# Optimization experiments

Measured on AMD Instinct MI355X. Metric: run time of the kernel, lower is better.

## Reference

```python
import math
import jax, jax.numpy as jnp
import numpy as np

HEADS = 9
EMBED = 32
TEMPERATURE = 3000.0

def _conv1x1(x, W, b):
    # x: [B,C,H,W], W: [O,C], b: [O]  (1x1 conv == channel matmul)
    return jnp.einsum('bchw,oc->bohw', x, W) + b[None, :, None, None]

def setup_inputs() -> dict:
    key = jax.random.key(0)
    ks = jax.random.split(key, 14)
    B, H, W = 2, 64, 64
    h2, w2 = 32, 32
    hd = HEADS * EMBED  # 288
    s = 0.1
    return {
        'second_frame': jax.random.normal(ks[0], (B, 3, H, W), jnp.float32),
        'first_frame_aligned': jax.random.normal(ks[1], (B, 3, H, W), jnp.float32),
        'second_frame_feat': jax.random.normal(ks[2], (B, 4, h2, w2), jnp.float32),
        'first_frame_feat_aligned': jax.random.normal(ks[3], (B, 4, h2, w2), jnp.float32),
        'Wq': jax.random.normal(ks[4], (hd, 3), jnp.float32) * s,
        'bq': jax.random.normal(ks[5], (hd,), jnp.float32) * s,
        'Wk': jax.random.normal(ks[6], (hd, 3), jnp.float32) * s,
        'bk': jax.random.normal(ks[7], (hd,), jnp.float32) * s,
        'Wv': jax.random.normal(ks[8], (hd, 4), jnp.float32) * s,
        'bv': jax.random.normal(ks[9], (hd,), jnp.float32) * s,
        'Wp': jax.random.normal(ks[10], (4, hd), jnp.float32) * s,
        'bp': jax.random.normal(ks[11], (4,), jnp.float32) * s,
        'Wt': jax.random.normal(ks[12], (1, EMBED), jnp.float32) * s,
        'bt': jax.random.normal(ks[13], (1,), jnp.float32) * s,
    }

def reference(second_frame, first_frame_aligned, second_frame_feat,
              first_frame_feat_aligned, Wq, bq, Wk, bk, Wv, bv, Wp, bp, Wt, bt):
    B, _, H, W = second_frame.shape
    HW = H * W
    # bilinear upsample of aligned features to (H, W); half-pixel centers == align_corners=False
    feat_up = jax.image.resize(first_frame_feat_aligned,
                               (B, first_frame_feat_aligned.shape[1], H, W),
                               method='linear', antialias=False)
    Q = _conv1x1(second_frame, Wq, bq).reshape(B, HEADS, EMBED, HW)
    K = _conv1x1(first_frame_aligned, Wk, bk).reshape(B, HEADS, EMBED, HW)
    V = _conv1x1(feat_up, Wv, bv).reshape(B, HEADS, EMBED, HW)
    Qn = jnp.transpose(Q, (0, 1, 3, 2))                      # [B,h,HW,d]
    sim = jnp.einsum('bhnd,bhdm->bhnm', Qn, K) / math.sqrt(EMBED)  # [B,h,HW,HW]
    # learned per-query threshold from Q
    t = jnp.einsum('bhnd,od->bhno', Qn, Wt) + bt             # [B,h,HW,1]
    attn = jax.nn.relu((sim - t) / TEMPERATURE)              # no row normalization
    out = jnp.einsum('bhnm,bhdm->bhnd', attn, V)             # [B,h,HW,d]
    out = jnp.transpose(out, (0, 1, 3, 2)).reshape(B, HEADS * EMBED, H, W)
    out_feat = _conv1x1(out, Wp, bp)                         # [B,4,H,W]
    h2, w2 = second_frame_feat.shape[-2:]
    out_feat_down = jax.image.resize(out_feat, (B, out_feat.shape[1], h2, w2),
                                     method='linear', antialias=False)
    final_feat = second_frame_feat + out_feat_down
    return final_feat, out_feat_down
```

## Files before the change

kernel.cpp:

```cpp
#include <hip/hip_runtime.h>
#include <hip/hip_bf16.h>
#include <cstddef>

#define NHEADS 9
#define D 32
#define SQ 4096
#define ZSPLIT 8
#define MBLK (SQ / ZSPLIT)
#define CHUNKS (MBLK / 64)
#define KROW 40
#define VROW 72

typedef __attribute__((ext_vector_type(8))) short bf16x8;
typedef __attribute__((ext_vector_type(4))) short bf16x4;
typedef __attribute__((ext_vector_type(4))) float f32x4;

__device__ __forceinline__ unsigned int f2bf(float f) {
    unsigned int u = __float_as_uint(f);
    u += 0x7fffu + ((u >> 16) & 1u);
    return u >> 16;
}

__device__ __forceinline__ void lds_barrier() {
    asm volatile("s_waitcnt lgkmcnt(0)\n\ts_barrier" ::: "memory");
}

__device__ __forceinline__ unsigned int trunc_pk(float lo, float hi) {
    return __builtin_amdgcn_perm(__float_as_uint(hi), __float_as_uint(lo),
                                 0x07060302u);
}

__device__ __forceinline__ bf16x8 relu_pack8(f32x4 s1, f32x4 s2) {
    const f32x4 zz = {0.f, 0.f, 0.f, 0.f};
    f32x4 a = __builtin_elementwise_max(s1, zz);
    f32x4 b = __builtin_elementwise_max(s2, zz);
    union { unsigned int u[4]; bf16x8 v; } P;
    P.u[0] = trunc_pk(a[0], a[1]);
    P.u[1] = trunc_pk(a[2], a[3]);
    P.u[2] = trunc_pk(b[0], b[1]);
    P.u[3] = trunc_pk(b[2], b[3]);
    return P.v;
}

__global__ __launch_bounds__(256) void prep_kernel(
    const float* __restrict__ x2, const float* __restrict__ x1,
    const float* __restrict__ feat1,
    const float* __restrict__ Wq, const float* __restrict__ bq,
    const float* __restrict__ Wk, const float* __restrict__ bk,
    const float* __restrict__ Wv, const float* __restrict__ bv,
    const float* __restrict__ Wt, const float* __restrict__ bt,
    unsigned short* __restrict__ Qb, unsigned short* __restrict__ Kb,
    unsigned short* __restrict__ Vt, float* __restrict__ tbuf,
    float* __restrict__ of)
{
    __shared__ unsigned short Vls[32 * 66];

    const int tid = threadIdx.x;
    int idx = blockIdx.x * blockDim.x + tid;
    if (idx < 2 * 4 * SQ) of[idx] = 0.0f;
    int g  = idx & 3;
    int nl = tid >> 2;
    int n  = (idx >> 2) & (SQ - 1);
    int bh = idx >> 14;
    int h  = bh % NHEADS;
    int b  = bh / NHEADS;

    float xs0 = x2[((size_t)b * 3 + 0) * SQ + n];
    float xs1 = x2[((size_t)b * 3 + 1) * SQ + n];
    float xs2 = x2[((size_t)b * 3 + 2) * SQ + n];
    float ys0 = x1[((size_t)b * 3 + 0) * SQ + n];
    float ys1 = x1[((size_t)b * 3 + 1) * SQ + n];
    float ys2 = x1[((size_t)b * 3 + 2) * SQ + n];

    int yy = n >> 6, xx = n & 63;
    int jy = yy >> 1, jx = xx >> 1;
    int j0, j1, i0, i1; float wy0, wy1, wx0, wx1;
    if (yy & 1) { j0 = jy; j1 = (jy < 31) ? jy + 1 : 31; wy0 = 0.75f; wy1 = 0.25f; }
    else        { j0 = (jy > 0) ? jy - 1 : 0; j1 = jy;   wy0 = 0.25f; wy1 = 0.75f; }
    if (xx & 1) { i0 = jx; i1 = (jx < 31) ? jx + 1 : 31; wx0 = 0.75f; wx1 = 0.25f; }
    else        { i0 = (jx > 0) ? jx - 1 : 0; i1 = jx;   wx0 = 0.25f; wx1 = 0.75f; }

    float fu[4];
#pragma unroll
    for (int c = 0; c < 4; ++c) {
        const float* f = feat1 + ((size_t)b * 4 + c) * 1024;
        fu[c] = wy0 * (wx0 * f[j0 * 32 + i0] + wx1 * f[j0 * 32 + i1]) +
                wy1 * (wx0 * f[j1 * 32 + i0] + wx1 * f[j1 * 32 + i1]);
    }

    const int d0 = g * 8;
    unsigned int qp[4], kp[4];
    float tpart = 0.0f;
#pragma unroll
    for (int j = 0; j < 8; ++j) {
        int d = d0 + j, hd = h * D + d;
        float q = bq[hd] + Wq[hd * 3] * xs0 + Wq[hd * 3 + 1] * xs1 + Wq[hd * 3 + 2] * xs2;
        float k = bk[hd] + Wk[hd * 3] * ys0 + Wk[hd * 3 + 1] * ys1 + Wk[hd * 3 + 2] * ys2;
        float v = bv[hd] + Wv[hd * 4] * fu[0] + Wv[hd * 4 + 1] * fu[1] +
                  Wv[hd * 4 + 2] * fu[2] + Wv[hd * 4 + 3] * fu[3];
        tpart += q * Wt[d];
        unsigned int qb_ = f2bf(q), kb_ = f2bf(k);
        if (j & 1) { qp[j >> 1] |= qb_ << 16; kp[j >> 1] |= kb_ << 16; }
        else       { qp[j >> 1]  = qb_;       kp[j >> 1]  = kb_; }
        Vls[d * 66 + nl] = (unsigned short)f2bf(v);
    }
    tpart += __shfl_xor(tpart, 1);
    tpart += __shfl_xor(tpart, 2);
    if (g == 0) tbuf[(size_t)bh * SQ + n] = tpart + bt[0];

    size_t base = ((size_t)bh * SQ + n) * D + d0;
    *(uint4*)(Qb + base) = make_uint4(qp[0], qp[1], qp[2], qp[3]);
    *(uint4*)(Kb + base) = make_uint4(kp[0], kp[1], kp[2], kp[3]);

    __syncthreads();
    {
        int r  = tid >> 3;
        int c4 = tid & 7;
        int n0 = (blockIdx.x & 63) * 64;
        unsigned int w0 = *(const unsigned int*)&Vls[r * 66 + c4 * 4];
        unsigned int w1 = *(const unsigned int*)&Vls[r * 66 + c4 * 4 + 2];
        *(uint2*)(Vt + ((size_t)bh * D + r) * SQ + n0 + c4 * 4) = make_uint2(w0, w1);
    }
}

#define COMPUTE(KS, VS)                                                          \
    {                                                                            \
        _Pragma("unroll")                                                        \
        for (int g32 = 0; g32 < 2; ++g32) {                                      \
            const unsigned short* kbase = KS + g32 * 32 * KROW;                  \
            bf16x8 kf1 = *(const bf16x8*)(kbase + l15 * KROW + quad * 8);        \
            bf16x8 kf2 = *(const bf16x8*)(kbase + (16 + l15) * KROW + quad * 8); \
            bf16x8 vlo = *(const bf16x8*)(VS + l15 * VROW + g32 * 32 + quad * 8);\
            bf16x8 vhi = *(const bf16x8*)(VS + (l15 + 16) * VROW + g32 * 32 + quad * 8);\
            f32x4 sA1 = __builtin_amdgcn_mfma_f32_16x16x32_bf16(kf1, qfA, ciA, 0, 0, 0);\
            f32x4 sA2 = __builtin_amdgcn_mfma_f32_16x16x32_bf16(kf2, qfA, ciA, 0, 0, 0);\
            f32x4 sB1 = __builtin_amdgcn_mfma_f32_16x16x32_bf16(kf1, qfB, ciB, 0, 0, 0);\
            f32x4 sB2 = __builtin_amdgcn_mfma_f32_16x16x32_bf16(kf2, qfB, ciB, 0, 0, 0);\
            f32x4 sC1 = __builtin_amdgcn_mfma_f32_16x16x32_bf16(kf1, qfC, ciC, 0, 0, 0);\
            f32x4 sC2 = __builtin_amdgcn_mfma_f32_16x16x32_bf16(kf2, qfC, ciC, 0, 0, 0);\
            f32x4 sD1 = __builtin_amdgcn_mfma_f32_16x16x32_bf16(kf1, qfD, ciD, 0, 0, 0);\
            f32x4 sD2 = __builtin_amdgcn_mfma_f32_16x16x32_bf16(kf2, qfD, ciD, 0, 0, 0);\
            bf16x8 pA = relu_pack8(sA1, sA2);                                    \
            bf16x8 pB = relu_pack8(sB1, sB2);                                    \
            bf16x8 pC = relu_pack8(sC1, sC2);                                    \
            bf16x8 pD = relu_pack8(sD1, sD2);                                    \
            accAl = __builtin_amdgcn_mfma_f32_16x16x32_bf16(vlo, pA, accAl, 0, 0, 0);\
            accAh = __builtin_amdgcn_mfma_f32_16x16x32_bf16(vhi, pA, accAh, 0, 0, 0);\
            accBl = __builtin_amdgcn_mfma_f32_16x16x32_bf16(vlo, pB, accBl, 0, 0, 0);\
            accBh = __builtin_amdgcn_mfma_f32_16x16x32_bf16(vhi, pB, accBh, 0, 0, 0);\
            accCl = __builtin_amdgcn_mfma_f32_16x16x32_bf16(vlo, pC, accCl, 0, 0, 0);\
            accCh = __builtin_amdgcn_mfma_f32_16x16x32_bf16(vhi, pC, accCh, 0, 0, 0);\
            accDl = __builtin_amdgcn_mfma_f32_16x16x32_bf16(vlo, pD, accDl, 0, 0, 0);\
            accDh = __builtin_amdgcn_mfma_f32_16x16x32_bf16(vhi, pD, accDh, 0, 0, 0);\
        }                                                                        \
    }

__global__ __launch_bounds__(256, 4) void attn_kernel(
    const unsigned short* __restrict__ Qb,
    const unsigned short* __restrict__ Kb,
    const unsigned short* __restrict__ Vt,
    const float* __restrict__ tbuf,
    const float* __restrict__ Wp,
    float* __restrict__ of)
{
    __shared__ __align__(16) unsigned short Ks0[64 * KROW];
    __shared__ __align__(16) unsigned short Ks1[64 * KROW];
    __shared__ __align__(16) unsigned short Vs0[32 * VROW];
    __shared__ __align__(16) unsigned short Vs1[32 * VROW];

    const int bh   = blockIdx.y;
    const int h    = bh % NHEADS;
    const int b    = bh / NHEADS;
    const int n0   = blockIdx.x * 256;
    const int mc0  = blockIdx.z * MBLK;
    const int tid  = threadIdx.x;
    const int wave = tid >> 6;
    const int lane = tid & 63;
    const int l15  = lane & 15;
    const int quad = lane >> 4;

    const int nw = n0 + wave * 64;

    const unsigned short* qbase = Qb + ((size_t)bh * SQ + nw + l15) * D + quad * 8;
    bf16x8 qfA = *(const bf16x8*)(qbase);
    bf16x8 qfB = *(const bf16x8*)(qbase + 16 * D);
    bf16x8 qfC = *(const bf16x8*)(qbase + 32 * D);
    bf16x8 qfD = *(const bf16x8*)(qbase + 48 * D);

    const float SQRT32 = 5.656854249492381f;
    const float* tb = tbuf + (size_t)bh * SQ + nw + l15;
    float TA = tb[0]  * SQRT32;
    float TB = tb[16] * SQRT32;
    float TC = tb[32] * SQRT32;
    float TD = tb[48] * SQRT32;
    const f32x4 ciA = {-TA, -TA, -TA, -TA};
    const f32x4 ciB = {-TB, -TB, -TB, -TB};
    const f32x4 ciC = {-TC, -TC, -TC, -TC};
    const f32x4 ciD = {-TD, -TD, -TD, -TD};

    const uint4* Kg4 = (const uint4*)(Kb + (size_t)bh * SQ * D);
    const uint4* Vg4 = (const uint4*)(Vt + (size_t)bh * D * SQ);

    const int krow = tid >> 2;
    const int kcol = (tid & 3) * 8;
    const int kslot = (krow & 32) + 4 * ((krow >> 3) & 3) + (krow & 3) + ((krow & 4) << 2);
    unsigned short* kdst0 = Ks0 + kslot * KROW + kcol;
    unsigned short* kdst1 = Ks1 + kslot * KROW + kcol;
    const int vd = tid >> 3;
    const int vm = (tid & 7) * 8;
    unsigned short* vdst0 = Vs0 + vd * VROW + vm;
    unsigned short* vdst1 = Vs1 + vd * VROW + vm;
    const int vgbase = vd * (SQ / 8) + (mc0 >> 3) + (tid & 7);

    f32x4 accAl = {0.f,0.f,0.f,0.f}, accAh = {0.f,0.f,0.f,0.f};
    f32x4 accBl = {0.f,0.f,0.f,0.f}, accBh = {0.f,0.f,0.f,0.f};
    f32x4 accCl = {0.f,0.f,0.f,0.f}, accCh = {0.f,0.f,0.f,0.f};
    f32x4 accDl = {0.f,0.f,0.f,0.f}, accDh = {0.f,0.f,0.f,0.f};

    {
        uint4 k0 = Kg4[(size_t)mc0 * 4 + tid];
        uint4 v0 = Vg4[vgbase];
        *(uint4*)kdst0 = k0;
        *(uint4*)vdst0 = v0;
    }
    uint4 kn = Kg4[(size_t)(mc0 + 64) * 4 + tid];
    uint4 vn = Vg4[vgbase + 8];
    lds_barrier();

#pragma unroll
    for (int c = 0; c < CHUNKS; c += 2) {
        COMPUTE(Ks0, Vs0);
        *(uint4*)kdst1 = kn;
        *(uint4*)vdst1 = vn;
        if (c + 2 < CHUNKS) {
            kn = Kg4[(size_t)(mc0 + (c + 2) * 64) * 4 + tid];
            vn = Vg4[vgbase + (c + 2) * 8];
        }
        lds_barrier();

        COMPUTE(Ks1, Vs1);
        if (c + 2 < CHUNKS) {
            *(uint4*)kdst0 = kn;
            *(uint4*)vdst0 = vn;
            kn = Kg4[(size_t)(mc0 + (c + 3) * 64) * 4 + tid];
            vn = Vg4[vgbase + (c + 3) * 8];
            lds_barrier();
        }
    }

    const float s1 = 5.892556509887896e-05f;
    const float* wph = Wp + h * D + quad * 4;
#pragma unroll
    for (int o = 0; o < 4; ++o) {
        float cA = 0.f, cB = 0.f, cC = 0.f, cD = 0.f;
#pragma unroll
        for (int r = 0; r < 4; ++r) {
            float wlo = wph[o * 288 + r], whi = wph[o * 288 + 16 + r];
            cA += accAl[r] * wlo + accAh[r] * whi;
            cB += accBl[r] * wlo + accBh[r] * whi;
            cC += accCl[r] * wlo + accCh[r] * whi;
            cD += accDl[r] * wlo + accDh[r] * whi;
        }
        cA += __shfl_xor(cA, 16); cA += __shfl_xor(cA, 32);
        cB += __shfl_xor(cB, 16); cB += __shfl_xor(cB, 32);
        cC += __shfl_xor(cC, 16); cC += __shfl_xor(cC, 32);
        cD += __shfl_xor(cD, 16); cD += __shfl_xor(cD, 32);
        if (quad == 0) {
            float* ob = &of[((size_t)b * 4 + o) * SQ + nw + l15];
            atomicAdd(ob,      cA * s1);
            atomicAdd(ob + 16, cB * s1);
            atomicAdd(ob + 32, cC * s1);
            atomicAdd(ob + 48, cD * s1);
        }
    }
}

__global__ void final_kernel(const float* __restrict__ of,
                             const float* __restrict__ sff,
                             const float* __restrict__ bp,
                             float* __restrict__ dout)
{
    int tid = blockIdx.x * blockDim.x + threadIdx.x;
    if (tid >= 8192) return;
    int i  = tid & 31;
    int jj = (tid >> 5) & 31;
    int bo = tid >> 10;
    int o  = bo & 3;
    const float* src = of + (size_t)bo * SQ;
    int y = jj * 2, x = i * 2;
    float dval = 0.25f * (src[y * 64 + x] + src[y * 64 + x + 1] +
                          src[(y + 1) * 64 + x] + src[(y + 1) * 64 + x + 1]) + bp[o];
    dout[tid]        = sff[tid] + dval;
    dout[8192 + tid] = dval;
}

extern "C" void kernel_launch(void* const* d_in, const int* in_sizes, int n_in,
                              void* d_out, int out_size, void* d_ws, size_t ws_size,
                              hipStream_t stream)
{
    const float* second_frame = (const float*)d_in[0];
    const float* first_frame  = (const float*)d_in[1];
    const float* sff          = (const float*)d_in[2];
    const float* ffa          = (const float*)d_in[3];
    const float* Wq = (const float*)d_in[4];
    const float* bq = (const float*)d_in[5];
    const float* Wk = (const float*)d_in[6];
    const float* bk = (const float*)d_in[7];
    const float* Wv = (const float*)d_in[8];
    const float* bv = (const float*)d_in[9];
    const float* Wp = (const float*)d_in[10];
    const float* bp = (const float*)d_in[11];
    const float* Wt = (const float*)d_in[12];
    const float* bt = (const float*)d_in[13];
    float* out = (float*)d_out;

    char* ws = (char*)d_ws;
    const size_t QKV = (size_t)2 * NHEADS * SQ * D * sizeof(unsigned short);
    unsigned short* Qb = (unsigned short*)ws;
    unsigned short* Kb = (unsigned short*)(ws + QKV);
    unsigned short* Vt = (unsigned short*)(ws + 2 * QKV);
    float* tbuf = (float*)(ws + 3 * QKV);
    float* of   = (float*)(ws + 3 * QKV + (size_t)2 * NHEADS * SQ * sizeof(float));

    prep_kernel<<<1152, 256, 0, stream>>>(second_frame, first_frame, ffa,
                                          Wq, bq, Wk, bk, Wv, bv, Wt, bt,
                                          Qb, Kb, Vt, tbuf, of);
    dim3 ag(16, 18, ZSPLIT);
    attn_kernel<<<ag, 256, 0, stream>>>(Qb, Kb, Vt, tbuf, Wp, of);
    final_kernel<<<32, 256, 0, stream>>>(of, sff, bp, out);
}
```

Baseline: 134.5 us.

## Remap attention grid for XCD locality, deepen prefetch, pack relu, set MFMA priority

Switches the attention launch to a 1D grid and remaps block indices so that blocks sharing the same head and key/value slice land on the same XCD, aiming for better L2 reuse of K/V. It deepens the register prefetch from one to two chunks ahead, so global load latency is covered across more compute. It also moves ReLU after the bf16 pack, using a packed integer max on the bf16 bits, and raises wave priority around the MFMA block. These add register pressure and redundant clamped loads at the tail, and the packed max on signed shorts relies on negative bf16 values sorting below zero.

```diff
diff --git a/kernel.cpp b/kernel.cpp
--- a/kernel.cpp
+++ b/kernel.cpp
@@ -31,15 +31,13 @@
 }
 
 __device__ __forceinline__ bf16x8 relu_pack8(f32x4 s1, f32x4 s2) {
-    const f32x4 zz = {0.f, 0.f, 0.f, 0.f};
-    f32x4 a = __builtin_elementwise_max(s1, zz);
-    f32x4 b = __builtin_elementwise_max(s2, zz);
     union { unsigned int u[4]; bf16x8 v; } P;
-    P.u[0] = trunc_pk(a[0], a[1]);
-    P.u[1] = trunc_pk(a[2], a[3]);
-    P.u[2] = trunc_pk(b[0], b[1]);
-    P.u[3] = trunc_pk(b[2], b[3]);
-    return P.v;
+    P.u[0] = trunc_pk(s1[0], s1[1]);
+    P.u[1] = trunc_pk(s1[2], s1[3]);
+    P.u[2] = trunc_pk(s2[0], s2[1]);
+    P.u[3] = trunc_pk(s2[2], s2[3]);
+    const bf16x8 z = {0, 0, 0, 0, 0, 0, 0, 0};
+    return __builtin_elementwise_max(P.v, z);
 }
 
 __global__ __launch_bounds__(256) void prep_kernel(
@@ -125,6 +123,7 @@
 
 #define COMPUTE(KS, VS)                                                          \
     {                                                                            \
+        __builtin_amdgcn_s_setprio(1);                                           \
         _Pragma("unroll")                                                        \
         for (int g32 = 0; g32 < 2; ++g32) {                                      \
             const unsigned short* kbase = KS + g32 * 32 * KROW;                  \
@@ -153,6 +152,7 @@
             accDl = __builtin_amdgcn_mfma_f32_16x16x32_bf16(vlo, pD, accDl, 0, 0, 0);\
             accDh = __builtin_amdgcn_mfma_f32_16x16x32_bf16(vhi, pD, accDh, 0, 0, 0);\
         }                                                                        \
+        __builtin_amdgcn_s_setprio(0);                                           \
     }
 
 __global__ __launch_bounds__(256, 4) void attn_kernel(
@@ -168,11 +168,18 @@
     __shared__ __align__(16) unsigned short Vs0[32 * VROW];
     __shared__ __align__(16) unsigned short Vs1[32 * VROW];
 
-    const int bh   = blockIdx.y;
+    const int lin  = blockIdx.x;
+    const int xcd  = lin & 7;
+    const int q8   = lin >> 3;
+    const int xblk = q8 & 15;
+    const int gl   = q8 >> 4;
+    const int grp  = xcd * 18 + gl;
+    const int bh   = grp >> 3;
+    const int zz   = grp & 7;
     const int h    = bh % NHEADS;
     const int b    = bh / NHEADS;
-    const int n0   = blockIdx.x * 256;
-    const int mc0  = blockIdx.z * MBLK;
+    const int n0   = xblk * 256;
+    const int mc0  = zz * MBLK;
     const int tid  = threadIdx.x;
     const int wave = tid >> 6;
     const int lane = tid & 63;
@@ -217,33 +224,35 @@
     f32x4 accCl = {0.f,0.f,0.f,0.f}, accCh = {0.f,0.f,0.f,0.f};
     f32x4 accDl = {0.f,0.f,0.f,0.f}, accDh = {0.f,0.f,0.f,0.f};
 
-    {
-        uint4 k0 = Kg4[(size_t)mc0 * 4 + tid];
-        uint4 v0 = Vg4[vgbase];
-        *(uint4*)kdst0 = k0;
-        *(uint4*)vdst0 = v0;
-    }
-    uint4 kn = Kg4[(size_t)(mc0 + 64) * 4 + tid];
-    uint4 vn = Vg4[vgbase + 8];
+    uint4 kA = Kg4[(size_t)mc0 * 4 + tid];
+    uint4 vA = Vg4[vgbase];
+    uint4 kB = Kg4[(size_t)(mc0 + 64) * 4 + tid];
+    uint4 vB = Vg4[vgbase + 8];
+    *(uint4*)kdst0 = kA;
+    *(uint4*)vdst0 = vA;
+    kA = Kg4[(size_t)(mc0 + 128) * 4 + tid];
+    vA = Vg4[vgbase + 16];
     lds_barrier();
 
 #pragma unroll
     for (int c = 0; c < CHUNKS; c += 2) {
         COMPUTE(Ks0, Vs0);
-        *(uint4*)kdst1 = kn;
-        *(uint4*)vdst1 = vn;
-        if (c + 2 < CHUNKS) {
-            kn = Kg4[(size_t)(mc0 + (c + 2) * 64) * 4 + tid];
-            vn = Vg4[vgbase + (c + 2) * 8];
+        *(uint4*)kdst1 = kB;
+        *(uint4*)vdst1 = vB;
+        {
+            const int nc = (c + 3 < CHUNKS) ? c + 3 : CHUNKS - 1;
+            kB = Kg4[(size_t)(mc0 + nc * 64) * 4 + tid];
+            vB = Vg4[vgbase + nc * 8];
         }
         lds_barrier();
 
         COMPUTE(Ks1, Vs1);
         if (c + 2 < CHUNKS) {
-            *(uint4*)kdst0 = kn;
-            *(uint4*)vdst0 = vn;
-            kn = Kg4[(size_t)(mc0 + (c + 3) * 64) * 4 + tid];
-            vn = Vg4[vgbase + (c + 3) * 8];
+            *(uint4*)kdst0 = kA;
+            *(uint4*)vdst0 = vA;
+            const int nc2 = (c + 4 < CHUNKS) ? c + 4 : CHUNKS - 1;
+            kA = Kg4[(size_t)(mc0 + nc2 * 64) * 4 + tid];
+            vA = Vg4[vgbase + nc2 * 8];
             lds_barrier();
         }
     }
@@ -325,7 +334,6 @@
     prep_kernel<<<1152, 256, 0, stream>>>(second_frame, first_frame, ffa,
                                           Wq, bq, Wk, bk, Wv, bv, Wt, bt,
                                           Qb, Kb, Vt, tbuf, of);
-    dim3 ag(16, 18, ZSPLIT);
-    attn_kernel<<<ag, 256, 0, stream>>>(Qb, Kb, Vt, tbuf, Wp, of);
+    attn_kernel<<<16 * 18 * ZSPLIT, 256, 0, stream>>>(Qb, Kb, Vt, tbuf, Wp, of);
     final_kernel<<<32, 256, 0, stream>>>(of, sff, bp, out);
 }
```

Result: slower. 144.4 us (+7.4%).
